# Optimization experiments

Measured on AMD Instinct MI355X. Metric: run time of the kernel, lower is better.

The kernel has to match this reference:

```python
import jax, jax.numpy as jnp
import numpy as np

NEG_SLOPE = 0.2


def setup_inputs() -> dict:
    key = jax.random.key(0)
    ks = jax.random.split(key, 7)
    N, E, F_IN, H, D = 100000, 1600000, 256, 4, 64
    feat = jax.random.normal(ks[0], (N, F_IN), dtype=jnp.float32)
    W = jax.random.normal(ks[1], (F_IN, H * D), dtype=jnp.float32) * (1.0 / np.sqrt(F_IN))
    attn_l = jax.random.normal(ks[2], (H, D), dtype=jnp.float32) * 0.1
    attn_r = jax.random.normal(ks[3], (H, D), dtype=jnp.float32) * 0.1
    bias = jnp.zeros((H * D,), dtype=jnp.float32)
    src = jax.random.randint(ks[4], (E,), 0, N, dtype=jnp.int32)
    dst = jax.random.randint(ks[5], (E,), 0, N, dtype=jnp.int32)
    return {"feat": feat, "W": W, "attn_l": attn_l, "attn_r": attn_r,
            "bias": bias, "src": src, "dst": dst}


def reference(feat, W, attn_l, attn_r, bias, src, dst):
    N = feat.shape[0]
    H, D = attn_l.shape
    # fc: [N, F_in] @ [F_in, H*D] -> [N, H, D]
    h = (feat @ W).reshape(N, H, D)
    # per-node attention logits (dot with attn vectors): [N, H]
    el = jnp.einsum('nhd,hd->nh', h, attn_l)
    er = jnp.einsum('nhd,hd->nh', h, attn_r)
    # edge scores: e_ij = LeakyReLU(el[src] + er[dst]) -> [E, H]
    e = el[src] + er[dst]
    e = jnp.where(e > 0, e, NEG_SLOPE * e)
    # segment softmax over destination neighborhoods
    e_max = jax.ops.segment_max(e, dst, num_segments=N)          # [N, H]
    e_max = jnp.where(jnp.isfinite(e_max), e_max, 0.0)           # guard 0-in-degree
    e_exp = jnp.exp(e - e_max[dst])                              # [E, H]
    denom = jax.ops.segment_sum(e_exp, dst, num_segments=N)      # [N, H]
    a = e_exp / jnp.maximum(denom[dst], 1e-16)                   # [E, H]
    # weighted scatter-add of source messages: [E, H, D] -> [N, H, D]
    msg = h[src] * a[:, :, None]
    out = jax.ops.segment_sum(msg, dst, num_segments=N)
    out = out + bias.reshape(1, H, D)
    return out
```

## Files before the change

### kernel.cpp

```cpp
#include <hip/hip_runtime.h>
#include <hip/hip_bf16.h>
#include <math.h>

#define HEADS 4
#define DHEAD 64
#define HD 256
#define F_IN 256
#define NEG_SLOPE 0.2f

typedef __attribute__((ext_vector_type(8))) short bf16x8;
typedef __attribute__((ext_vector_type(8))) ushort u16x8;
typedef __attribute__((ext_vector_type(4))) float f32x4;

__device__ __forceinline__ ushort f2bf(float f) {
    __hip_bfloat16 b = __float2bfloat16(f);
    ushort u; __builtin_memcpy(&u, &b, 2);
    return u;
}

#define HIST_BLOCKS 3072
__global__ __launch_bounds__(256) void prep_k(const float* __restrict__ W,
                                              ushort* __restrict__ Wt,
                                              const int* __restrict__ dst,
                                              int* __restrict__ counts,
                                              ushort* __restrict__ pos, int E) {
    if (blockIdx.x < 256) {
        int i = blockIdx.x * 256 + threadIdx.x;
        int k = i >> 8, c = i & 255;
        int ct = c >> 4, kb = k >> 5, kh = (k >> 3) & 3, j = k & 7;
        int l = kh * 16 + (c & 15);
        Wt[(size_t)((ct * 8 + kb) * 64 + l) * 8 + j] = f2bf(W[i]);
    } else {
        const int stride = HIST_BLOCKS * 256;
        for (int i = (blockIdx.x - 256) * 256 + threadIdx.x; i < E; i += stride)
            pos[i] = (ushort)atomicAdd(&counts[dst[i]], 1);
    }
}

__global__ __launch_bounds__(256) void gemm_k(const float* __restrict__ A,
                                              const ushort* __restrict__ Wt,
                                              const float* __restrict__ attn_l,
                                              const float* __restrict__ attn_r,
                                              ushort* __restrict__ hbf,
                                              float* __restrict__ el,
                                              float* __restrict__ er, int M) {
    __shared__ ushort As[64 * 256];
    const int tid = threadIdx.x;
    const int wave = tid >> 6;
    const int lane = tid & 63;
    const int r16 = lane & 15;
    const int khalf = lane >> 4;
    const int row0 = blockIdx.x * 64;
    const int wcol0 = wave * 64;

    bf16x8 b[4][8];
#pragma unroll
    for (int nc = 0; nc < 4; ++nc) {
        const int ct = wave * 4 + nc;
#pragma unroll
        for (int kb = 0; kb < 8; ++kb)
            b[nc][kb] = *(const bf16x8*)(Wt + ((size_t)(ct * 8 + kb) * 64 + lane) * 8);
    }

    {
        const int srow = tid >> 2;
        const int cg = tid & 3;
        int arow = row0 + srow; if (arow >= M) arow = M - 1;
        const float* ap = A + (size_t)arow * F_IN + cg * 64;
        const int sw = (srow & 7) << 4;
        char* wb = (char*)As + srow * 512;
#pragma unroll
        for (int q = 0; q < 8; ++q) {
            float4 f0 = *(const float4*)(ap + q * 8);
            float4 f1 = *(const float4*)(ap + q * 8 + 4);
            u16x8 cv;
            cv[0] = f2bf(f0.x); cv[1] = f2bf(f0.y); cv[2] = f2bf(f0.z); cv[3] = f2bf(f0.w);
            cv[4] = f2bf(f1.x); cv[5] = f2bf(f1.y); cv[6] = f2bf(f1.z); cv[7] = f2bf(f1.w);
            *(u16x8*)(wb + ((cg * 128 + q * 16) ^ sw)) = cv;
        }
    }
    __syncthreads();

    f32x4 acc[4][4] = {};
#pragma unroll
    for (int kb = 0; kb < 8; ++kb) {
        bf16x8 a[4];
#pragma unroll
        for (int mr = 0; mr < 4; ++mr) {
            const int row = mr * 16 + r16;
            const int sw = (row & 7) << 4;
            a[mr] = *(const bf16x8*)((const char*)As + row * 512 +
                                     ((kb * 64 + khalf * 16) ^ sw));
        }
#pragma unroll
        for (int mr = 0; mr < 4; ++mr)
#pragma unroll
            for (int nc = 0; nc < 4; ++nc)
                acc[mr][nc] = __builtin_amdgcn_mfma_f32_16x16x32_bf16(
                    a[mr], b[nc][kb], acc[mr][nc], 0, 0, 0);
    }

    float al[4], ar[4];
#pragma unroll
    for (int nc = 0; nc < 4; ++nc) {
        al[nc] = attn_l[wcol0 + nc * 16 + r16];
        ar[nc] = attn_r[wcol0 + nc * 16 + r16];
    }
#pragma unroll
    for (int mr = 0; mr < 4; ++mr) {
#pragma unroll
        for (int r = 0; r < 4; ++r) {
            int row = row0 + mr * 16 + khalf * 4 + r;
            float vl = 0.f, vr = 0.f;
#pragma unroll
            for (int nc = 0; nc < 4; ++nc) {
                float v = acc[mr][nc][r];
                vl = fmaf(v, al[nc], vl);
                vr = fmaf(v, ar[nc], vr);
            }
#pragma unroll
            for (int off = 1; off < 16; off <<= 1) {
                vl += __shfl_xor(vl, off);
                vr += __shfl_xor(vr, off);
            }
            if (row < M) {
                if (r16 == 0) {
                    el[row * HEADS + wave] = vl;
                    er[row * HEADS + wave] = vr;
                }
#pragma unroll
                for (int nc = 0; nc < 4; ++nc)
                    hbf[(size_t)row * HD + wcol0 + nc * 16 + r16] = f2bf(acc[mr][nc][r]);
            }
        }
    }
}

#define SCAN_SPAN 4096
__global__ __launch_bounds__(1024) void blocksum_k(const int* __restrict__ counts,
                                                   int* __restrict__ btot, int N) {
    __shared__ int wsum[16];
    const int tid = threadIdx.x, lane = tid & 63, wid = tid >> 6;
    int i0 = blockIdx.x * SCAN_SPAN + tid * 4;
    int t = 0;
#pragma unroll
    for (int r = 0; r < 4; ++r) { int i = i0 + r; if (i < N) t += counts[i]; }
#pragma unroll
    for (int off = 32; off; off >>= 1) t += __shfl_xor(t, off);
    if (lane == 0) wsum[wid] = t;
    __syncthreads();
    if (tid == 0) {
        int s = 0;
        for (int w = 0; w < 16; ++w) s += wsum[w];
        btot[blockIdx.x] = s;
    }
}

__global__ __launch_bounds__(64) void scanb_k(const int* __restrict__ btot,
                                              int* __restrict__ boff, int nb) {
    int lane = threadIdx.x;
    int v = (lane < nb) ? btot[lane] : 0;
    int sc = v;
    for (int off = 1; off < 64; off <<= 1) {
        int u = __shfl_up(sc, off);
        if (lane >= off) sc += u;
    }
    if (lane < nb) boff[lane] = sc - v;
}

__global__ __launch_bounds__(1024) void scanw_k(const int* __restrict__ counts,
                                                const int* __restrict__ boff,
                                                int* __restrict__ row_start, int N) {
    __shared__ int wsum[16];
    const int tid = threadIdx.x, lane = tid & 63, wid = tid >> 6;
    int i0 = blockIdx.x * SCAN_SPAN + tid * 4;
    int v[4]; int t = 0;
#pragma unroll
    for (int r = 0; r < 4; ++r) { int i = i0 + r; v[r] = (i < N) ? counts[i] : 0; t += v[r]; }
    int sc = t;
    for (int off = 1; off < 64; off <<= 1) {
        int u = __shfl_up(sc, off);
        if (lane >= off) sc += u;
    }
    if (lane == 63) wsum[wid] = sc;
    __syncthreads();
    int wpref = 0;
    for (int w = 0; w < wid; ++w) wpref += wsum[w];
    int excl = boff[blockIdx.x] + wpref + sc - t;
    int run = 0;
#pragma unroll
    for (int r = 0; r < 4; ++r) {
        int i = i0 + r;
        if (i < N) row_start[i] = excl + run;
        run += v[r];
    }
    if (N - 1 >= i0 && N - 1 < i0 + 4) row_start[N] = excl + run;
}

__global__ __launch_bounds__(256) void place_k(const int* __restrict__ src,
                                               const int* __restrict__ dst,
                                               const ushort* __restrict__ pos,
                                               const int* __restrict__ row_start,
                                               int* __restrict__ sorted_src, int E) {
    int i = blockIdx.x * 256 + threadIdx.x;
    if (i < E)
        sorted_src[row_start[dst[i]] + (int)pos[i]] = src[i];
}

__global__ __launch_bounds__(256) void gat4_k(const ushort* __restrict__ hbf,
                                              const float* __restrict__ el,
                                              const float* __restrict__ er,
                                              const float* __restrict__ bias,
                                              const int* __restrict__ row_start,
                                              const int* __restrict__ sorted_src,
                                              float* __restrict__ out, int N) {
    __shared__ int   s_idx[4][64];
    __shared__ float p_s[4][64][4];
    const int wv = threadIdx.x >> 6, lane = threadIdx.x & 63;
    const int head = lane >> 4;
    const int n = blockIdx.x * 4 + wv;
    if (n >= N) return;

    const int start = row_start[n], end = row_start[n + 1];
    const int deg = end - start;

    const float4 er4 = *(const float4*)&er[n * 4];
    const ushort* __restrict__ hrow = hbf + (unsigned)lane * 4u;

    float acc0 = 0.f, acc1 = 0.f, acc2 = 0.f, acc3 = 0.f, ssum = 0.f;

#define GLOAD(i, V, Q) { int s_ = s_idx[wv][i]; Q = p_s[wv][i][head]; \
                         V = *(const uint2*)(hrow + (size_t)(unsigned)s_ * HD); }
#define GUSE(V, Q) { union { unsigned u; float f; } b0_, b1_, b2_, b3_; \
                     b0_.u = V.x << 16; b1_.u = V.x & 0xffff0000u; \
                     b2_.u = V.y << 16; b3_.u = V.y & 0xffff0000u; \
                     acc0 = fmaf(Q, b0_.f, acc0); acc1 = fmaf(Q, b1_.f, acc1); \
                     acc2 = fmaf(Q, b2_.f, acc2); acc3 = fmaf(Q, b3_.f, acc3); \
                     ssum += Q; }

    for (int c0 = 0; c0 < deg; c0 += 64) {
        const int cnt = min(64, deg - c0);
        if (lane < cnt) {
            int s = sorted_src[start + c0 + lane];
            float4 e4 = *(const float4*)&el[s * 4];
            float4 pv;
            float x0 = e4.x + er4.x; x0 = fmaxf(x0, NEG_SLOPE * x0);
            float x1 = e4.y + er4.y; x1 = fmaxf(x1, NEG_SLOPE * x1);
            float x2 = e4.z + er4.z; x2 = fmaxf(x2, NEG_SLOPE * x2);
            float x3 = e4.w + er4.w; x3 = fmaxf(x3, NEG_SLOPE * x3);
            pv.x = __expf(x0); pv.y = __expf(x1); pv.z = __expf(x2); pv.w = __expf(x3);
            s_idx[wv][lane] = s;
            *(float4*)&p_s[wv][lane][0] = pv;
        }
        __builtin_amdgcn_wave_barrier();

        int k = 0;
        if (cnt >= 16) {
            uint2 V[8]; float Q[8];
#pragma unroll
            for (int j = 0; j < 8; ++j) GLOAD(j, V[j], Q[j]);
            for (; k + 16 <= cnt; k += 8) {
#pragma unroll
                for (int j = 0; j < 8; ++j) { GUSE(V[j], Q[j]); GLOAD(k + 8 + j, V[j], Q[j]); }
            }
#pragma unroll
            for (int j = 0; j < 8; ++j) GUSE(V[j], Q[j]);
            k += 8;
        } else if (cnt >= 8) {
            uint2 va, vb, vc, vd; float qa, qb, qc, qd;
            GLOAD(0, va, qa); GLOAD(1, vb, qb); GLOAD(2, vc, qc); GLOAD(3, vd, qd);
            for (; k + 8 <= cnt; k += 4) {
                GUSE(va, qa); GLOAD(k + 4, va, qa);
                GUSE(vb, qb); GLOAD(k + 5, vb, qb);
                GUSE(vc, qc); GLOAD(k + 6, vc, qc);
                GUSE(vd, qd); GLOAD(k + 7, vd, qd);
            }
            GUSE(va, qa); GUSE(vb, qb); GUSE(vc, qc); GUSE(vd, qd);
            k += 4;
        }
        for (; k < cnt; ++k) { uint2 v; float q; GLOAD(k, v, q); GUSE(v, q); }
        __builtin_amdgcn_wave_barrier();
    }
#undef GLOAD
#undef GUSE

    const float inv = 1.0f / fmaxf(ssum, 1e-16f);
    const float4 b4 = *(const float4*)&bias[lane * 4];
    float4 o;
    o.x = fmaf(acc0, inv, b4.x);
    o.y = fmaf(acc1, inv, b4.y);
    o.z = fmaf(acc2, inv, b4.z);
    o.w = fmaf(acc3, inv, b4.w);
    *(float4*)&out[(size_t)n * HD + lane * 4] = o;
}

extern "C" void kernel_launch(void* const* d_in, const int* in_sizes, int n_in,
                              void* d_out, int out_size, void* d_ws, size_t ws_size,
                              hipStream_t stream) {
    const float* feat   = (const float*)d_in[0];
    const float* W      = (const float*)d_in[1];
    const float* attn_l = (const float*)d_in[2];
    const float* attn_r = (const float*)d_in[3];
    const float* bias   = (const float*)d_in[4];
    const int*   src    = (const int*)d_in[5];
    const int*   dst    = (const int*)d_in[6];

    const int N = in_sizes[0] / F_IN;
    const int E = in_sizes[5];

    ushort* hbf = (ushort*)d_ws;
    float* el = (float*)(hbf + (size_t)N * HD);
    float* er = el + (size_t)N * HEADS;
    int* counts     = (int*)(er + (size_t)N * HEADS);
    int* row_start  = counts + N;
    int* sorted_src = row_start + (N + 1);
    int* btot       = sorted_src + E;
    int* boff       = btot + 64;
    ushort* pos     = (ushort*)(boff + 64);
    ushort* Wt = (ushort*)(((uintptr_t)(pos + E) + 15) & ~(uintptr_t)15);

    float* out = (float*)d_out;

    const int nb = (N + SCAN_SPAN - 1) / SCAN_SPAN;

    hipMemsetAsync(counts, 0, (size_t)N * sizeof(int), stream);
    prep_k<<<256 + HIST_BLOCKS, 256, 0, stream>>>(W, Wt, dst, counts, pos, E);
    gemm_k<<<(N + 63) / 64, 256, 0, stream>>>(feat, Wt, attn_l, attn_r, hbf, el, er, N);

    blocksum_k<<<nb, 1024, 0, stream>>>(counts, btot, N);
    scanb_k<<<1, 64, 0, stream>>>(btot, boff, nb);
    scanw_k<<<nb, 1024, 0, stream>>>(counts, boff, row_start, N);
    place_k<<<(E + 255) / 256, 256, 0, stream>>>(src, dst, pos, row_start, sorted_src, E);

    gat4_k<<<(N + 3) / 4, 256, 0, stream>>>(hbf, el, er, bias, row_start, sorted_src, out, N);
}
```

Measured before the change: 320.3 us.

## Fuse degree histogram into GEMM kernel and convert W in-register

Merges the W-to-bf16 prep and destination-degree histogram into the GEMM launch: GEMM blocks now read fp32 W directly with strided loads and convert in registers, while extra blocks perform the atomic histogram concurrently. This removes one kernel launch and the Wt staging buffer and lets histogram atomics overlap with GEMM work. It also reduces histogram block count and drops the 8-deep load pipeline in the aggregation kernel in favor of the 4-deep path, which may reduce register pressure but lowers memory-level parallelism for high-degree nodes. Each GEMM block now redundantly loads and converts W with uncoalesced scalar loads.

```diff
diff --git a/kernel.cpp b/kernel.cpp
--- a/kernel.cpp
+++ b/kernel.cpp
@@ -18,33 +18,27 @@
     return u;
 }
 
-#define HIST_BLOCKS 3072
-__global__ __launch_bounds__(256) void prep_k(const float* __restrict__ W,
-                                              ushort* __restrict__ Wt,
-                                              const int* __restrict__ dst,
-                                              int* __restrict__ counts,
-                                              ushort* __restrict__ pos, int E) {
-    if (blockIdx.x < 256) {
-        int i = blockIdx.x * 256 + threadIdx.x;
-        int k = i >> 8, c = i & 255;
-        int ct = c >> 4, kb = k >> 5, kh = (k >> 3) & 3, j = k & 7;
-        int l = kh * 16 + (c & 15);
-        Wt[(size_t)((ct * 8 + kb) * 64 + l) * 8 + j] = f2bf(W[i]);
-    } else {
+#define HIST_BLOCKS 2048
+__global__ __launch_bounds__(256) void fused_k(const float* __restrict__ A,
+                                               const float* __restrict__ W,
+                                               const float* __restrict__ attn_l,
+                                               const float* __restrict__ attn_r,
+                                               ushort* __restrict__ hbf,
+                                               float* __restrict__ el,
+                                               float* __restrict__ er,
+                                               const int* __restrict__ dst,
+                                               int* __restrict__ counts,
+                                               ushort* __restrict__ pos,
+                                               int M, int E, int GB) {
+    __shared__ ushort As[64 * 256];
+
+    if (blockIdx.x >= GB) {
         const int stride = HIST_BLOCKS * 256;
-        for (int i = (blockIdx.x - 256) * 256 + threadIdx.x; i < E; i += stride)
+        for (int i = (blockIdx.x - GB) * 256 + threadIdx.x; i < E; i += stride)
             pos[i] = (ushort)atomicAdd(&counts[dst[i]], 1);
-    }
-}
-
-__global__ __launch_bounds__(256) void gemm_k(const float* __restrict__ A,
-                                              const ushort* __restrict__ Wt,
-                                              const float* __restrict__ attn_l,
-                                              const float* __restrict__ attn_r,
-                                              ushort* __restrict__ hbf,
-                                              float* __restrict__ el,
-                                              float* __restrict__ er, int M) {
-    __shared__ ushort As[64 * 256];
+        return;
+    }
+
     const int tid = threadIdx.x;
     const int wave = tid >> 6;
     const int lane = tid & 63;
@@ -56,10 +50,14 @@
     bf16x8 b[4][8];
 #pragma unroll
     for (int nc = 0; nc < 4; ++nc) {
-        const int ct = wave * 4 + nc;
-#pragma unroll
-        for (int kb = 0; kb < 8; ++kb)
-            b[nc][kb] = *(const bf16x8*)(Wt + ((size_t)(ct * 8 + kb) * 64 + lane) * 8);
+#pragma unroll
+        for (int kb = 0; kb < 8; ++kb) {
+            const float* wp = W + (size_t)(kb * 32 + khalf * 8) * HD + wcol0 + nc * 16 + r16;
+            union { u16x8 u; bf16x8 h; } cv;
+#pragma unroll
+            for (int j = 0; j < 8; ++j) cv.u[j] = f2bf(wp[(size_t)j * HD]);
+            b[nc][kb] = cv.h;
+        }
     }
 
     {
@@ -255,18 +253,7 @@
         __builtin_amdgcn_wave_barrier();
 
         int k = 0;
-        if (cnt >= 16) {
-            uint2 V[8]; float Q[8];
-#pragma unroll
-            for (int j = 0; j < 8; ++j) GLOAD(j, V[j], Q[j]);
-            for (; k + 16 <= cnt; k += 8) {
-#pragma unroll
-                for (int j = 0; j < 8; ++j) { GUSE(V[j], Q[j]); GLOAD(k + 8 + j, V[j], Q[j]); }
-            }
-#pragma unroll
-            for (int j = 0; j < 8; ++j) GUSE(V[j], Q[j]);
-            k += 8;
-        } else if (cnt >= 8) {
+        if (cnt >= 8) {
             uint2 va, vb, vc, vd; float qa, qb, qc, qd;
             GLOAD(0, va, qa); GLOAD(1, vb, qb); GLOAD(2, vc, qc); GLOAD(3, vd, qd);
             for (; k + 8 <= cnt; k += 4) {
@@ -317,15 +304,15 @@
     int* btot       = sorted_src + E;
     int* boff       = btot + 64;
     ushort* pos     = (ushort*)(boff + 64);
-    ushort* Wt = (ushort*)(((uintptr_t)(pos + E) + 15) & ~(uintptr_t)15);
 
     float* out = (float*)d_out;
 
     const int nb = (N + SCAN_SPAN - 1) / SCAN_SPAN;
+    const int GB = (N + 63) / 64;
 
     hipMemsetAsync(counts, 0, (size_t)N * sizeof(int), stream);
-    prep_k<<<256 + HIST_BLOCKS, 256, 0, stream>>>(W, Wt, dst, counts, pos, E);
-    gemm_k<<<(N + 63) / 64, 256, 0, stream>>>(feat, Wt, attn_l, attn_r, hbf, el, er, N);
+    fused_k<<<GB + HIST_BLOCKS, 256, 0, stream>>>(feat, W, attn_l, attn_r,
+                                                  hbf, el, er, dst, counts, pos, N, E, GB);
 
     blocksum_k<<<nb, 1024, 0, stream>>>(counts, btot, N);
     scanb_k<<<1, 64, 0, stream>>>(btot, boff, nb);
```

After: 326.8 us. 1.02x slower.
